# Performance work log

Hardware: AMD Instinct MI355X
Metric: run time of the kernel (lower is better)

The kernel has to match this reference:

```python
import jax, jax.numpy as jnp
import numpy as np

NUM_CLASSES = 21
IOU_THRESH = 0.5
NEG_POS_RATIO = 3
VAR0, VAR1 = 0.1, 0.2


def point_form(priors):
    # (cx,cy,w,h) -> (xmin,ymin,xmax,ymax)
    return jnp.concatenate([priors[:, :2] - priors[:, 2:] / 2,
                            priors[:, :2] + priors[:, 2:] / 2], axis=-1)


def jaccard(box_a, box_b):
    # box_a: [n,4] point form, box_b: [N,4] point form -> [n,N]
    max_xy = jnp.minimum(box_a[:, None, 2:], box_b[None, :, 2:])
    min_xy = jnp.maximum(box_a[:, None, :2], box_b[None, :, :2])
    inter = jnp.prod(jnp.clip(max_xy - min_xy, 0.0, None), axis=-1)
    area_a = jnp.prod(box_a[:, 2:] - box_a[:, :2], axis=-1)[:, None]
    area_b = jnp.prod(box_b[:, 2:] - box_b[:, :2], axis=-1)[None, :]
    return inter / (area_a + area_b - inter)


def encode(matched, priors):
    # matched: [N,4] point form, priors: [N,4] center form
    g_cxcy = ((matched[:, :2] + matched[:, 2:]) / 2 - priors[:, :2]) / (VAR0 * priors[:, 2:])
    g_wh = jnp.log((matched[:, 2:] - matched[:, :2]) / priors[:, 2:]) / VAR1
    return jnp.concatenate([g_cxcy, g_wh], axis=-1)


def match_one(truths, labels, priors):
    # truths: [n_obj,4], labels: [n_obj], priors: [N,4] center form
    ov = jaccard(truths, point_form(priors))          # [n_obj, N]
    best_prior_idx = jnp.argmax(ov, axis=1)           # [n_obj]
    best_truth_overlap = jnp.max(ov, axis=0)          # [N]
    best_truth_idx = jnp.argmax(ov, axis=0)           # [N]
    best_truth_overlap = best_truth_overlap.at[best_prior_idx].set(2.0)
    def body(j, bti):
        return bti.at[best_prior_idx[j]].set(j)
    best_truth_idx = jax.lax.fori_loop(0, truths.shape[0], body, best_truth_idx)
    matched = truths[best_truth_idx]                  # [N,4]
    conf = labels[best_truth_idx].astype(jnp.int32) + 1
    conf = jnp.where(best_truth_overlap < IOU_THRESH, 0, conf)
    return encode(matched, priors), conf


def smooth_l1(x):
    ax = jnp.abs(x)
    return jnp.where(ax < 1.0, 0.5 * x * x, ax - 0.5)


def setup_inputs() -> dict:
    key = jax.random.key(0)
    k1, k2, k3, k4, k5, k6, k7 = jax.random.split(key, 7)
    B, N, n_obj = 128, 8732, 16
    loc_data = jax.random.normal(k1, (B, N, 4), jnp.float32)
    conf_data = jax.random.normal(k2, (B, N, NUM_CLASSES), jnp.float32)
    # valid ground-truth boxes in [0,1], point form, plus class label in [0,20)
    mins = jax.random.uniform(k3, (B, n_obj, 2)) * 0.6
    sizes = jax.random.uniform(k4, (B, n_obj, 2)) * 0.35 + 0.05
    labels = jax.random.randint(k5, (B, n_obj), 0, NUM_CLASSES - 1).astype(jnp.float32)
    targets = jnp.concatenate([mins, mins + sizes, labels[..., None]], axis=-1)
    # priors in center form with positive w,h
    centers = jax.random.uniform(k6, (N, 2))
    wh = jax.random.uniform(k7, (N, 2)) * 0.5 + 0.05
    priors = jnp.concatenate([centers, wh], axis=-1).astype(jnp.float32)
    return {"loc_data": loc_data, "conf_data": conf_data, "targets": targets, "priors": priors}


def _forward(loc_data, conf_data, targets, priors):
    B, N = loc_data.shape[0], loc_data.shape[1]
    truths, labels = targets[:, :, :4], targets[:, :, 4]
    target_loc, target_conf = jax.vmap(match_one, in_axes=(0, 0, None))(truths, labels, priors)
    pos = target_conf > 0                             # [B,N]
    # localization: smooth-L1 summed over positive priors
    loss_l = jnp.sum(smooth_l1(loc_data - target_loc) * pos[..., None].astype(loc_data.dtype))
    # per-prior CE surrogate: logsumexp - logit[target]
    lse = jax.nn.logsumexp(conf_data, axis=-1)        # [B,N]
    gathered = jnp.take_along_axis(conf_data, target_conf[..., None], axis=-1)[..., 0]
    loss_c_all = lse - gathered                       # [B,N]
    # hard negative mining via double argsort ranking (positives excluded)
    lc = jnp.where(pos, 0.0, loss_c_all)
    loss_idx = jnp.argsort(-lc, axis=1)
    idx_rank = jnp.argsort(loss_idx, axis=1)
    num_pos = jnp.sum(pos.astype(jnp.int32), axis=1, keepdims=True)   # [B,1]
    num_neg = jnp.minimum(NEG_POS_RATIO * num_pos, N - 1)
    neg = idx_rank < num_neg
    sel = pos | neg
    loss_c = jnp.sum(jnp.where(sel, loss_c_all, 0.0))
    n_total = jnp.sum(num_pos).astype(loc_data.dtype)
    return loss_l / n_total, loss_c / n_total


def reference(loc_data, conf_data, targets, priors):
    return _forward(loc_data, conf_data, targets, priors)
```

## Files before the change

### kernel.cpp

```cpp
#include <hip/hip_runtime.h>
#include <cstdint>
#include <cstddef>

#define HB1 4096
#define HB2 2048
#define CMAX 21
#define IOU_T 0.5f

__device__ __forceinline__ float sl1(float x) {
    float ax = fabsf(x);
    return ax < 1.0f ? 0.5f * x * x : ax - 0.5f;
}

__global__ __launch_bounds__(256) void kA_best_prior(
    const float* __restrict__ targets, const float* __restrict__ priors,
    float* __restrict__ bpi_val, int* __restrict__ bpi_idx,
    int* __restrict__ num_pos_g, float* __restrict__ accB_g,
    float* __restrict__ acc_g, unsigned* __restrict__ done_g,
    int N, int NOBJ, int SLICES, int CHUNK, int B)
{
    const int s = blockIdx.x, b = blockIdx.y, t = threadIdx.x;
    __shared__ float tb[16 * 4];
    __shared__ float ta[16];
    __shared__ float wv[4 * 16];
    __shared__ int   wi[4 * 16];

    if (s == 0 && b == 0) {
        for (int q = t; q < B; q += 256) num_pos_g[q] = 0;
        for (int q = t; q < 2 * B; q += 256) accB_g[q] = 0.f;
        if (t < 4) acc_g[t] = 0.f;
        if (t == 0) *done_g = 0u;
    }

    if (t < 16) {
        if (t < NOBJ) {
            const float* tr = targets + ((size_t)b * NOBJ + t) * 5;
            float x0 = tr[0], y0 = tr[1], x1 = tr[2], y1 = tr[3];
            tb[t * 4 + 0] = x0; tb[t * 4 + 1] = y0;
            tb[t * 4 + 2] = x1; tb[t * 4 + 3] = y1;
            ta[t] = (x1 - x0) * (y1 - y0);
        } else {
            tb[t * 4 + 0] = 0.f; tb[t * 4 + 1] = 0.f;
            tb[t * 4 + 2] = 0.f; tb[t * 4 + 3] = 0.f;
            ta[t] = 0.f;
        }
    }
    __syncthreads();

    float bv[16]; int bi[16];
#pragma unroll
    for (int j = 0; j < 16; j++) { bv[j] = -1.0f; bi[j] = 0x7fffffff; }

    const int start = s * CHUNK;
    const int end = min(start + CHUNK, N);
    for (int i = start + t; i < end; i += 256) {
        float4 p = ((const float4*)priors)[i];
        float bx0 = p.x - p.z * 0.5f, by0 = p.y - p.w * 0.5f;
        float bx1 = p.x + p.z * 0.5f, by1 = p.y + p.w * 0.5f;
        float ab = (bx1 - bx0) * (by1 - by0);
#pragma unroll
        for (int j = 0; j < 16; j++) {
            float iw = fminf(tb[j * 4 + 2], bx1) - fmaxf(tb[j * 4 + 0], bx0);
            float ih = fminf(tb[j * 4 + 3], by1) - fmaxf(tb[j * 4 + 1], by0);
            iw = fmaxf(iw, 0.f); ih = fmaxf(ih, 0.f);
            float inter = iw * ih;
            float iou = inter / (ta[j] + ab - inter);
            if (iou > bv[j] || (iou == bv[j] && i < bi[j])) { bv[j] = iou; bi[j] = i; }
        }
    }

#pragma unroll
    for (int off = 32; off >= 1; off >>= 1) {
#pragma unroll
        for (int j = 0; j < 16; j++) {
            float v2 = __shfl_down(bv[j], off, 64);
            int   i2 = __shfl_down(bi[j], off, 64);
            if (v2 > bv[j] || (v2 == bv[j] && i2 < bi[j])) { bv[j] = v2; bi[j] = i2; }
        }
    }
    const int wid = t >> 6, lane = t & 63;
    if (lane == 0) {
#pragma unroll
        for (int j = 0; j < 16; j++) { wv[wid * 16 + j] = bv[j]; wi[wid * 16 + j] = bi[j]; }
    }
    __syncthreads();
    if (t < 16) {
        float v = wv[t]; int idx = wi[t];
#pragma unroll
        for (int w = 1; w < 4; w++) {
            float v2 = wv[w * 16 + t]; int i2 = wi[w * 16 + t];
            if (v2 > v || (v2 == v && i2 < idx)) { v = v2; idx = i2; }
        }
        if (t < NOBJ) {
            int o = (b * SLICES + s) * 16 + t;
            bpi_val[o] = v;
            bpi_idx[o] = idx;
        }
    }
}

#define IOU_STEP(j) { \
    float4 tj = tb4[j]; \
    float taj = (tj.z - tj.x) * (tj.w - tj.y); \
    float iw = fminf(tj.z, bx1) - fmaxf(tj.x, bx0); \
    float ih = fminf(tj.w, by1) - fmaxf(tj.y, by0); \
    iw = fmaxf(iw, 0.f); ih = fmaxf(ih, 0.f); \
    float inter = iw * ih; \
    float iou = inter * __builtin_amdgcn_rcpf(taj + ab - inter); \
    if (iou > bto) { bto = iou; bti = (j); } }

__global__ __launch_bounds__(256, 3) void kB_main(
    const float* __restrict__ loc, const float* __restrict__ conf,
    const float* __restrict__ targets, const float* __restrict__ priors,
    const float* __restrict__ bpi_val, const int* __restrict__ bpi_idx,
    float* __restrict__ lc_out, int* __restrict__ num_pos, float* __restrict__ accB,
    int N, int NOBJ, int SLICES, int TPB, int BPB)
{
    const int g = blockIdx.x;
    const int b = g / BPB;
    const int j0 = g % BPB;
    const int t = threadIdx.x;
    const int wid = t >> 6, lane = t & 63;

    __shared__ __align__(16) float buf[256 * CMAX];
    __shared__ __align__(16) float tb[16 * 4];
    __shared__ float tl[16];
    __shared__ __align__(16) int bpi_s[16];
    __shared__ float wred[4 * 3];

    if (t < 16) {
        if (t < NOBJ) {
            const float* tr = targets + ((size_t)b * NOBJ + t) * 5;
            tb[t * 4 + 0] = tr[0]; tb[t * 4 + 1] = tr[1];
            tb[t * 4 + 2] = tr[2]; tb[t * 4 + 3] = tr[3];
            tl[t] = tr[4];
            float bv = -1.f; int bi = 0x7fffffff;
            for (int s2 = 0; s2 < SLICES; s2++) {
                int o = (b * SLICES + s2) * 16 + t;
                float v = bpi_val[o]; int idx = bpi_idx[o];
                if (v > bv || (v == bv && idx < bi)) { bv = v; bi = idx; }
            }
            bpi_s[t] = bi;
        } else {
            tb[t * 4 + 0] = 0.f; tb[t * 4 + 1] = 0.f; tb[t * 4 + 2] = 0.f; tb[t * 4 + 3] = 0.f;
            tl[t] = 0.f; bpi_s[t] = -1;
        }
    }

    const float* confB = conf + (size_t)b * N * CMAX;
    const float* locB  = loc + (size_t)b * N * 4;

    float4 r0, r1, r2, r3, r4, r5, pld, ppr;

    auto stage = [&](int xx) {
        int i0s = xx * 256;
        int rows_s = min(256, N - i0s);
        int nf4s = (rows_s * CMAX) >> 2;
        const float4* s4 = (const float4*)(confB + (size_t)i0s * CMAX);
        if (t + 0    < nf4s) r0 = s4[t + 0];
        if (t + 256  < nf4s) r1 = s4[t + 256];
        if (t + 512  < nf4s) r2 = s4[t + 512];
        if (t + 768  < nf4s) r3 = s4[t + 768];
        if (t + 1024 < nf4s) r4 = s4[t + 1024];
        if (t + 1280 < nf4s) r5 = s4[t + 1280];
        if (t < rows_s) {
            ppr = ((const float4*)priors)[i0s + t];
            pld = ((const float4*)locB)[i0s + t];
        }
    };

    float ll = 0.f, plc = 0.f, np = 0.f;
    int x = j0;
    if (x < TPB) stage(x);

    while (x < TPB) {
        const int i0 = x * 256;
        const int rows = min(256, N - i0);
        const int nf4 = (rows * CMAX) >> 2;

        __syncthreads();

        float4 myp = ppr, myl = pld;
        float4* bp4f = (float4*)buf;
        if (t + 0    < nf4) bp4f[t + 0]    = r0;
        if (t + 256  < nf4) bp4f[t + 256]  = r1;
        if (t + 512  < nf4) bp4f[t + 512]  = r2;
        if (t + 768  < nf4) bp4f[t + 768]  = r3;
        if (t + 1024 < nf4) bp4f[t + 1024] = r4;
        if (t + 1280 < nf4) bp4f[t + 1280] = r5;
        __syncthreads();

        int xn = x + BPB;
        if (xn < TPB) stage(xn);

        if (t < rows) {
            const int i = i0 + t;
            float4 pp = myp;
            float bx0 = pp.x - pp.z * 0.5f, by0 = pp.y - pp.w * 0.5f;
            float bx1 = pp.x + pp.z * 0.5f, by1 = pp.y + pp.w * 0.5f;
            float ab = (bx1 - bx0) * (by1 - by0);
            float bto = -1.f; int bti = 0;
            const float4* tb4 = (const float4*)tb;
            if (NOBJ == 16) {
#pragma unroll
                for (int j = 0; j < 16; j++) IOU_STEP(j);
            } else {
                for (int j = 0; j < NOBJ; j++) IOU_STEP(j);
            }
            const int4* bp4 = (const int4*)bpi_s;
#pragma unroll
            for (int jj = 0; jj < 4; jj++) {
                int4 q = bp4[jj];
                if (q.x == i) { bto = 2.0f; bti = jj * 4 + 0; }
                if (q.y == i) { bto = 2.0f; bti = jj * 4 + 1; }
                if (q.z == i) { bto = 2.0f; bti = jj * 4 + 2; }
                if (q.w == i) { bto = 2.0f; bti = jj * 4 + 3; }
            }
            bool pos = !(bto < IOU_T);
            if (pos) {
                float4 tj = tb4[bti];
                float rz = __builtin_amdgcn_rcpf(pp.z);
                float rw = __builtin_amdgcn_rcpf(pp.w);
                float gcx = ((tj.x + tj.z) * 0.5f - pp.x) * (10.0f * rz);
                float gcy = ((tj.y + tj.w) * 0.5f - pp.y) * (10.0f * rw);
                float gw = __logf((tj.z - tj.x) * rz) * 5.0f;
                float gh = __logf((tj.w - tj.y) * rw) * 5.0f;
                ll += sl1(myl.x - gcx) + sl1(myl.y - gcy) + sl1(myl.z - gw) + sl1(myl.w - gh);
                np += 1.f;
            }
            int cf = pos ? ((int)tl[bti] + 1) : 0;
            const float* cr = buf + t * CMAX;
            float m = cr[0];
#pragma unroll
            for (int c = 1; c < CMAX; c++) m = fmaxf(m, cr[c]);
            float ssum = 0.f;
#pragma unroll
            for (int c = 0; c < CMAX; c++) ssum += __expf(cr[c] - m);
            float lse = m + __logf(ssum);
            float lossc = lse - cr[cf];
            if (pos) plc += lossc;
            float lcv = pos ? 0.f : lossc;
            lcv = fmaxf(lcv, 0.f);
            lc_out[(size_t)b * N + i] = lcv;
        }
        x = xn;
    }

#pragma unroll
    for (int off = 32; off >= 1; off >>= 1) {
        ll  += __shfl_down(ll, off, 64);
        plc += __shfl_down(plc, off, 64);
        np  += __shfl_down(np, off, 64);
    }
    if (lane == 0) { wred[wid * 3 + 0] = ll; wred[wid * 3 + 1] = plc; wred[wid * 3 + 2] = np; }
    __syncthreads();
    if (t == 0) {
        float a0 = 0.f, a1 = 0.f, a2 = 0.f;
#pragma unroll
        for (int w = 0; w < 4; w++) { a0 += wred[w * 3 + 0]; a1 += wred[w * 3 + 1]; a2 += wred[w * 3 + 2]; }
        atomicAdd(&accB[b * 2 + 0], a0);
        atomicAdd(&accB[b * 2 + 1], a1);
        atomicAdd(&num_pos[b], (int)a2);
    }
}

__device__ __forceinline__ void wave_sufscan(int& c, float& s, int lane) {
#pragma unroll
    for (int off = 1; off < 64; off <<= 1) {
        int c2 = __shfl_down(c, off, 64);
        float s2 = __shfl_down(s, off, 64);
        if (lane + off < 64) { c += c2; s += s2; }
    }
}

__global__ __launch_bounds__(1024) void kC_topk(
    const float* __restrict__ lc, const int* __restrict__ num_pos,
    const float* __restrict__ accB,
    float* __restrict__ acc, unsigned* __restrict__ done_ctr,
    float* __restrict__ out, int N, int B)
{
    const int b = blockIdx.x, t = threadIdx.x;
    const int NT = 1024;
    const int wid = t >> 6, lane = t & 63;
    __shared__ __align__(16) int   cnt[HB1];
    __shared__ __align__(16) float sm[HB1];
    __shared__ int   wc[16];
    __shared__ float ws[16];
    __shared__ int s_strad, s_krem;
    __shared__ float s_above;
    __shared__ int s_last;
    __shared__ float wsum[16], wsA[16], wsB[16];

    const int k = min(3 * num_pos[b], N - 1);
    const float* lcb = lc + (size_t)b * N;
    float total = 0.f;

    if (k > 0) {
        ((int4*)cnt)[t] = make_int4(0, 0, 0, 0);
        ((float4*)sm)[t] = make_float4(0.f, 0.f, 0.f, 0.f);
        __syncthreads();
        const int n4 = N >> 2;
        const float4* lcb4 = (const float4*)lcb;
        for (int i = t; i < n4; i += NT) {
            float4 v = lcb4[i];
            { unsigned u = __float_as_uint(v.x) >> 19; atomicAdd(&cnt[u], 1); atomicAdd(&sm[u], v.x); }
            { unsigned u = __float_as_uint(v.y) >> 19; atomicAdd(&cnt[u], 1); atomicAdd(&sm[u], v.y); }
            { unsigned u = __float_as_uint(v.z) >> 19; atomicAdd(&cnt[u], 1); atomicAdd(&sm[u], v.z); }
            { unsigned u = __float_as_uint(v.w) >> 19; atomicAdd(&cnt[u], 1); atomicAdd(&sm[u], v.w); }
        }
        for (int i = (n4 << 2) + t; i < N; i += NT) {
            float v = lcb[i];
            unsigned u = __float_as_uint(v) >> 19;
            atomicAdd(&cnt[u], 1); atomicAdd(&sm[u], v);
        }
        __syncthreads();
        {
            int4  cv = ((const int4*)cnt)[t];
            float4 sv = ((const float4*)sm)[t];
            int   ci = cv.x + cv.y + cv.z + cv.w;
            float si = sv.x + sv.y + sv.z + sv.w;
            wave_sufscan(ci, si, lane);
            if (lane == 0) { wc[wid] = ci; ws[wid] = si; }
            __syncthreads();
            int cab = 0; float sab = 0.f;
            for (int w = wid + 1; w < 16; w++) { cab += wc[w]; sab += ws[w]; }
            int   i0c = ci + cab;          float f0 = si + sab;
            int   i1c = i0c - cv.x;        float f1 = f0 - sv.x;
            int   i2c = i1c - cv.y;        float f2 = f1 - sv.y;
            int   i3c = i2c - cv.z;        float f3 = f2 - sv.z;
            int   i4c = i3c - cv.w;
            if (i1c < k && k <= i0c) { s_strad = 4 * t + 0; s_krem = k - i1c; s_above = f1; }
            if (i2c < k && k <= i1c) { s_strad = 4 * t + 1; s_krem = k - i2c; s_above = f2; }
            if (i3c < k && k <= i2c) { s_strad = 4 * t + 2; s_krem = k - i3c; s_above = f3; }
            if (i4c < k && k <= i3c) { s_strad = 4 * t + 3; s_krem = k - i4c; s_above = f3 - sv.w; }
        }
        __syncthreads();
        const int s1 = s_strad, k2 = s_krem;
        total += s_above;

        __syncthreads();
        ((int2*)cnt)[t] = make_int2(0, 0);
        ((float2*)sm)[t] = make_float2(0.f, 0.f);
        __syncthreads();
        for (int i = t; i < N; i += NT) {
            float v = lcb[i];
            unsigned u = __float_as_uint(v);
            if ((int)(u >> 19) == s1) {
                int q = (int)((u >> 8) & 0x7FF);
                atomicAdd(&cnt[q], 1); atomicAdd(&sm[q], v);
            }
        }
        __syncthreads();
        {
            int2  cv = ((const int2*)cnt)[t];
            float2 sv = ((const float2*)sm)[t];
            int   ci = cv.x + cv.y;
            float si = sv.x + sv.y;
            wave_sufscan(ci, si, lane);
            if (lane == 0) { wc[wid] = ci; ws[wid] = si; }
            __syncthreads();
            int cab = 0; float sab = 0.f;
            for (int w = wid + 1; w < 16; w++) { cab += wc[w]; sab += ws[w]; }
            int   i0c = ci + cab;       float f0 = si + sab;
            int   i1c = i0c - cv.x;     float f1 = f0 - sv.x;
            int   i2c = i1c - cv.y;
            if (i1c < k2 && k2 <= i0c) { s_strad = 2 * t + 0; s_krem = k2 - i1c; s_above = f1; }
            if (i2c < k2 && k2 <= i1c) { s_strad = 2 * t + 1; s_krem = k2 - i2c; s_above = f1 - sv.y; }
        }
        __syncthreads();
        const int s2 = s_strad, krem = s_krem;
        total += s_above;
        float tval = __uint_as_float((((unsigned)s1) << 19) | (((unsigned)s2) << 8));
        total += (float)krem * tval;
    }

    if (t == 0) {
        if (k > 0) atomicAdd(&acc[1], total);
        __threadfence();
        unsigned old = atomicAdd(done_ctr, 1u);
        s_last = (old == (unsigned)gridDim.x - 1u) ? 1 : 0;
    }
    __syncthreads();
    if (s_last) {
        __threadfence();
        float vn = 0.f, va = 0.f, vb = 0.f;
        for (int q = t; q < B; q += NT) {
            vn += (float)num_pos[q];
            va += accB[q * 2 + 0];
            vb += accB[q * 2 + 1];
        }
#pragma unroll
        for (int off = 32; off >= 1; off >>= 1) {
            vn += __shfl_down(vn, off, 64);
            va += __shfl_down(va, off, 64);
            vb += __shfl_down(vb, off, 64);
        }
        if (lane == 0) { wsum[wid] = vn; wsA[wid] = va; wsB[wid] = vb; }
        __syncthreads();
        if (t == 0) {
            float n = 0.f, a = 0.f, bsum = 0.f;
#pragma unroll
            for (int w = 0; w < 16; w++) { n += wsum[w]; a += wsA[w]; bsum += wsB[w]; }
            float l2 = atomicAdd(&acc[1], 0.0f);
            out[0] = a / n;
            out[1] = (bsum + l2) / n;
        }
    }
}

extern "C" void kernel_launch(void* const* d_in, const int* in_sizes, int n_in,
                              void* d_out, int out_size, void* d_ws, size_t ws_size,
                              hipStream_t stream)
{
    const float* loc     = (const float*)d_in[0];
    const float* conf    = (const float*)d_in[1];
    const float* targets = (const float*)d_in[2];
    const float* priors  = (const float*)d_in[3];
    float* out = (float*)d_out;

    const int N = in_sizes[3] / 4;
    const int BN = in_sizes[0] / 4;
    const int B = BN / N;
    const int NOBJ = in_sizes[2] / (B * 5);
    const int SLICES = 8;
    const int CHUNK = (N + SLICES - 1) / SLICES;
    const int TPB = (N + 255) / 256;
    const int BPB = 14;

    char* w = (char*)d_ws;
    float*    lc_ws   = (float*)w;                         size_t off = (size_t)BN * 4;
    float*    bpi_val = (float*)(w + off);                 off += (size_t)B * SLICES * 16 * 4;
    int*      bpi_idx = (int*)(w + off);                   off += (size_t)B * SLICES * 16 * 4;
    int*      num_pos = (int*)(w + off);                   off += (size_t)B * 4;
    float*    accB    = (float*)(w + off);                 off += (size_t)B * 2 * 4;
    float*    acc     = (float*)(w + off);                 off += 16;
    unsigned* done    = (unsigned*)(w + off);              off += 16;

    dim3 gA(SLICES, B);
    kA_best_prior<<<gA, 256, 0, stream>>>(targets, priors, bpi_val, bpi_idx,
                                          num_pos, accB, acc, done, N, NOBJ, SLICES, CHUNK, B);

    kB_main<<<B * BPB, 256, 0, stream>>>(loc, conf, targets, priors, bpi_val, bpi_idx,
                                         lc_ws, num_pos, accB, N, NOBJ, SLICES, TPB, BPB);

    kC_topk<<<B, 1024, 0, stream>>>(lc_ws, num_pos, accB, acc, done, out, N, B);
}
```

Baseline: 228.7 us.

## Fuse top-k selection into main kernel via per-batch last-block completion counter

The separate histogram-based top-k kernel is merged into the main loss kernel. The last of the BPB blocks of each batch row, found through an atomic per-batch counter, runs the two-pass radix selection with 256 threads instead of 1024. This removes one kernel launch and the gap between launches, and lets selection for one row overlap with main work on other rows. The change also lowers BPB from 14 to 8, raises the occupancy hint to 4 blocks per CU, and puts shared memory into a 32KB union. The tail work per row now runs on a single 256-thread block, so that serial stage may get longer.

After: 390.4 us. 70.7% more time.

```diff
diff --git a/kernel.cpp b/kernel.cpp
--- a/kernel.cpp
+++ b/kernel.cpp
@@ -2,8 +2,6 @@
 #include <cstdint>
 #include <cstddef>
 
-#define HB1 4096
-#define HB2 2048
 #define CMAX 21
 #define IOU_T 0.5f
 
@@ -17,6 +15,7 @@
     float* __restrict__ bpi_val, int* __restrict__ bpi_idx,
     int* __restrict__ num_pos_g, float* __restrict__ accB_g,
     float* __restrict__ acc_g, unsigned* __restrict__ done_g,
+    int* __restrict__ bdone_g,
     int N, int NOBJ, int SLICES, int CHUNK, int B)
 {
     const int s = blockIdx.x, b = blockIdx.y, t = threadIdx.x;
@@ -28,6 +27,7 @@
     if (s == 0 && b == 0) {
         for (int q = t; q < B; q += 256) num_pos_g[q] = 0;
         for (int q = t; q < 2 * B; q += 256) accB_g[q] = 0.f;
+        for (int q = t; q < B; q += 256) bdone_g[q] = 0;
         if (t < 4) acc_g[t] = 0.f;
         if (t == 0) *done_g = 0u;
     }
@@ -99,6 +99,15 @@
     }
 }
 
+__device__ __forceinline__ void wave_sufscan(int& c, float& s, int lane) {
+#pragma unroll
+    for (int off = 1; off < 64; off <<= 1) {
+        int c2 = __shfl_down(c, off, 64);
+        float s2 = __shfl_down(s, off, 64);
+        if (lane + off < 64) { c += c2; s += s2; }
+    }
+}
+
 #define IOU_STEP(j) { \
     float4 tj = tb4[j]; \
     float taj = (tj.z - tj.x) * (tj.w - tj.y); \
@@ -109,12 +118,19 @@
     float iou = inter * __builtin_amdgcn_rcpf(taj + ab - inter); \
     if (iou > bto) { bto = iou; bti = (j); } }
 
-__global__ __launch_bounds__(256, 3) void kB_main(
+#define CSTEP(idx, cc, ff, kk) { \
+    int nc = curc - (cc); float nf = curf - (ff); \
+    if (nc < (kk) && (kk) <= curc) { s_strad = (idx); s_krem = (kk) - nc; s_above = nf; } \
+    curc = nc; curf = nf; }
+
+__global__ __launch_bounds__(256, 4) void kBC_main(
     const float* __restrict__ loc, const float* __restrict__ conf,
     const float* __restrict__ targets, const float* __restrict__ priors,
     const float* __restrict__ bpi_val, const int* __restrict__ bpi_idx,
     float* __restrict__ lc_out, int* __restrict__ num_pos, float* __restrict__ accB,
-    int N, int NOBJ, int SLICES, int TPB, int BPB)
+    int* __restrict__ bdone, float* __restrict__ acc, unsigned* __restrict__ done_ctr,
+    float* __restrict__ out,
+    int N, int NOBJ, int SLICES, int TPB, int BPB, int B)
 {
     const int g = blockIdx.x;
     const int b = g / BPB;
@@ -122,11 +138,20 @@
     const int t = threadIdx.x;
     const int wid = t >> 6, lane = t & 63;
 
-    __shared__ __align__(16) float buf[256 * CMAX];
+    __shared__ __align__(16) char smem[32768];
     __shared__ __align__(16) float tb[16 * 4];
     __shared__ float tl[16];
     __shared__ __align__(16) int bpi_s[16];
     __shared__ float wred[4 * 3];
+    __shared__ int s_go;
+    __shared__ int wc[4];
+    __shared__ float ws[4];
+    __shared__ int s_strad, s_krem;
+    __shared__ float s_above;
+    __shared__ int s_last;
+    __shared__ float wsum[4], wsA[4], wsB[4];
+
+    float* buf = (float*)smem;
 
     if (t < 16) {
         if (t < NOBJ) {
@@ -262,87 +287,80 @@
         atomicAdd(&accB[b * 2 + 1], a1);
         atomicAdd(&num_pos[b], (int)a2);
     }
-}
-
-__device__ __forceinline__ void wave_sufscan(int& c, float& s, int lane) {
-#pragma unroll
-    for (int off = 1; off < 64; off <<= 1) {
-        int c2 = __shfl_down(c, off, 64);
-        float s2 = __shfl_down(s, off, 64);
-        if (lane + off < 64) { c += c2; s += s2; }
-    }
-}
-
-__global__ __launch_bounds__(1024) void kC_topk(
-    const float* __restrict__ lc, const int* __restrict__ num_pos,
-    const float* __restrict__ accB,
-    float* __restrict__ acc, unsigned* __restrict__ done_ctr,
-    float* __restrict__ out, int N, int B)
-{
-    const int b = blockIdx.x, t = threadIdx.x;
-    const int NT = 1024;
-    const int wid = t >> 6, lane = t & 63;
-    __shared__ __align__(16) int   cnt[HB1];
-    __shared__ __align__(16) float sm[HB1];
-    __shared__ int   wc[16];
-    __shared__ float ws[16];
-    __shared__ int s_strad, s_krem;
-    __shared__ float s_above;
-    __shared__ int s_last;
-    __shared__ float wsum[16], wsA[16], wsB[16];
-
+
+    __threadfence();
+    if (t == 0) {
+        int old = atomicAdd(&bdone[b], 1);
+        s_go = (old == BPB - 1) ? 1 : 0;
+    }
+    __syncthreads();
+    if (!s_go) return;
+    __threadfence();
+
+    int*   cnt = (int*)smem;
+    float* sm  = (float*)(smem + 16384);
     const int k = min(3 * num_pos[b], N - 1);
-    const float* lcb = lc + (size_t)b * N;
+    const float* lcb = lc_out + (size_t)b * N;
     float total = 0.f;
 
     if (k > 0) {
-        ((int4*)cnt)[t] = make_int4(0, 0, 0, 0);
-        ((float4*)sm)[t] = make_float4(0.f, 0.f, 0.f, 0.f);
+#pragma unroll
+        for (int q = 0; q < 4; q++) {
+            ((int4*)cnt)[t + 256 * q] = make_int4(0, 0, 0, 0);
+            ((float4*)sm)[t + 256 * q] = make_float4(0.f, 0.f, 0.f, 0.f);
+        }
         __syncthreads();
         const int n4 = N >> 2;
         const float4* lcb4 = (const float4*)lcb;
-        for (int i = t; i < n4; i += NT) {
+        for (int i = t; i < n4; i += 256) {
             float4 v = lcb4[i];
             { unsigned u = __float_as_uint(v.x) >> 19; atomicAdd(&cnt[u], 1); atomicAdd(&sm[u], v.x); }
             { unsigned u = __float_as_uint(v.y) >> 19; atomicAdd(&cnt[u], 1); atomicAdd(&sm[u], v.y); }
             { unsigned u = __float_as_uint(v.z) >> 19; atomicAdd(&cnt[u], 1); atomicAdd(&sm[u], v.z); }
             { unsigned u = __float_as_uint(v.w) >> 19; atomicAdd(&cnt[u], 1); atomicAdd(&sm[u], v.w); }
         }
-        for (int i = (n4 << 2) + t; i < N; i += NT) {
+        for (int i = (n4 << 2) + t; i < N; i += 256) {
             float v = lcb[i];
             unsigned u = __float_as_uint(v) >> 19;
             atomicAdd(&cnt[u], 1); atomicAdd(&sm[u], v);
         }
         __syncthreads();
         {
-            int4  cv = ((const int4*)cnt)[t];
-            float4 sv = ((const float4*)sm)[t];
-            int   ci = cv.x + cv.y + cv.z + cv.w;
-            float si = sv.x + sv.y + sv.z + sv.w;
+            int4   cv0 = ((const int4*)cnt)[4 * t + 0], cv1 = ((const int4*)cnt)[4 * t + 1];
+            int4   cv2 = ((const int4*)cnt)[4 * t + 2], cv3 = ((const int4*)cnt)[4 * t + 3];
+            float4 sv0 = ((const float4*)sm)[4 * t + 0], sv1 = ((const float4*)sm)[4 * t + 1];
+            float4 sv2 = ((const float4*)sm)[4 * t + 2], sv3 = ((const float4*)sm)[4 * t + 3];
+            int ci = cv0.x + cv0.y + cv0.z + cv0.w + cv1.x + cv1.y + cv1.z + cv1.w
+                   + cv2.x + cv2.y + cv2.z + cv2.w + cv3.x + cv3.y + cv3.z + cv3.w;
+            float si = sv0.x + sv0.y + sv0.z + sv0.w + sv1.x + sv1.y + sv1.z + sv1.w
+                     + sv2.x + sv2.y + sv2.z + sv2.w + sv3.x + sv3.y + sv3.z + sv3.w;
             wave_sufscan(ci, si, lane);
             if (lane == 0) { wc[wid] = ci; ws[wid] = si; }
             __syncthreads();
             int cab = 0; float sab = 0.f;
-            for (int w = wid + 1; w < 16; w++) { cab += wc[w]; sab += ws[w]; }
-            int   i0c = ci + cab;          float f0 = si + sab;
-            int   i1c = i0c - cv.x;        float f1 = f0 - sv.x;
-            int   i2c = i1c - cv.y;        float f2 = f1 - sv.y;
-            int   i3c = i2c - cv.z;        float f3 = f2 - sv.z;
-            int   i4c = i3c - cv.w;
-            if (i1c < k && k <= i0c) { s_strad = 4 * t + 0; s_krem = k - i1c; s_above = f1; }
-            if (i2c < k && k <= i1c) { s_strad = 4 * t + 1; s_krem = k - i2c; s_above = f2; }
-            if (i3c < k && k <= i2c) { s_strad = 4 * t + 2; s_krem = k - i3c; s_above = f3; }
-            if (i4c < k && k <= i3c) { s_strad = 4 * t + 3; s_krem = k - i4c; s_above = f3 - sv.w; }
+            for (int w = wid + 1; w < 4; w++) { cab += wc[w]; sab += ws[w]; }
+            int curc = ci + cab; float curf = si + sab;
+            const int base = 16 * t;
+            CSTEP(base + 0,  cv0.x, sv0.x, k) CSTEP(base + 1,  cv0.y, sv0.y, k)
+            CSTEP(base + 2,  cv0.z, sv0.z, k) CSTEP(base + 3,  cv0.w, sv0.w, k)
+            CSTEP(base + 4,  cv1.x, sv1.x, k) CSTEP(base + 5,  cv1.y, sv1.y, k)
+            CSTEP(base + 6,  cv1.z, sv1.z, k) CSTEP(base + 7,  cv1.w, sv1.w, k)
+            CSTEP(base + 8,  cv2.x, sv2.x, k) CSTEP(base + 9,  cv2.y, sv2.y, k)
+            CSTEP(base + 10, cv2.z, sv2.z, k) CSTEP(base + 11, cv2.w, sv2.w, k)
+            CSTEP(base + 12, cv3.x, sv3.x, k) CSTEP(base + 13, cv3.y, sv3.y, k)
+            CSTEP(base + 14, cv3.z, sv3.z, k) CSTEP(base + 15, cv3.w, sv3.w, k)
         }
         __syncthreads();
         const int s1 = s_strad, k2 = s_krem;
         total += s_above;
 
         __syncthreads();
-        ((int2*)cnt)[t] = make_int2(0, 0);
-        ((float2*)sm)[t] = make_float2(0.f, 0.f);
-        __syncthreads();
-        for (int i = t; i < N; i += NT) {
+        ((int4*)cnt)[t] = make_int4(0, 0, 0, 0);
+        ((int4*)cnt)[t + 256] = make_int4(0, 0, 0, 0);
+        ((float4*)sm)[t] = make_float4(0.f, 0.f, 0.f, 0.f);
+        ((float4*)sm)[t + 256] = make_float4(0.f, 0.f, 0.f, 0.f);
+        __syncthreads();
+        for (int i = t; i < N; i += 256) {
             float v = lcb[i];
             unsigned u = __float_as_uint(v);
             if ((int)(u >> 19) == s1) {
@@ -352,20 +370,21 @@
         }
         __syncthreads();
         {
-            int2  cv = ((const int2*)cnt)[t];
-            float2 sv = ((const float2*)sm)[t];
-            int   ci = cv.x + cv.y;
-            float si = sv.x + sv.y;
+            int4   cv0 = ((const int4*)cnt)[2 * t + 0], cv1 = ((const int4*)cnt)[2 * t + 1];
+            float4 sv0 = ((const float4*)sm)[2 * t + 0], sv1 = ((const float4*)sm)[2 * t + 1];
+            int ci = cv0.x + cv0.y + cv0.z + cv0.w + cv1.x + cv1.y + cv1.z + cv1.w;
+            float si = sv0.x + sv0.y + sv0.z + sv0.w + sv1.x + sv1.y + sv1.z + sv1.w;
             wave_sufscan(ci, si, lane);
             if (lane == 0) { wc[wid] = ci; ws[wid] = si; }
             __syncthreads();
             int cab = 0; float sab = 0.f;
-            for (int w = wid + 1; w < 16; w++) { cab += wc[w]; sab += ws[w]; }
-            int   i0c = ci + cab;       float f0 = si + sab;
-            int   i1c = i0c - cv.x;     float f1 = f0 - sv.x;
-            int   i2c = i1c - cv.y;
-            if (i1c < k2 && k2 <= i0c) { s_strad = 2 * t + 0; s_krem = k2 - i1c; s_above = f1; }
-            if (i2c < k2 && k2 <= i1c) { s_strad = 2 * t + 1; s_krem = k2 - i2c; s_above = f1 - sv.y; }
+            for (int w = wid + 1; w < 4; w++) { cab += wc[w]; sab += ws[w]; }
+            int curc = ci + cab; float curf = si + sab;
+            const int base = 8 * t;
+            CSTEP(base + 0, cv0.x, sv0.x, k2) CSTEP(base + 1, cv0.y, sv0.y, k2)
+            CSTEP(base + 2, cv0.z, sv0.z, k2) CSTEP(base + 3, cv0.w, sv0.w, k2)
+            CSTEP(base + 4, cv1.x, sv1.x, k2) CSTEP(base + 5, cv1.y, sv1.y, k2)
+            CSTEP(base + 6, cv1.z, sv1.z, k2) CSTEP(base + 7, cv1.w, sv1.w, k2)
         }
         __syncthreads();
         const int s2 = s_strad, krem = s_krem;
@@ -378,13 +397,13 @@
         if (k > 0) atomicAdd(&acc[1], total);
         __threadfence();
         unsigned old = atomicAdd(done_ctr, 1u);
-        s_last = (old == (unsigned)gridDim.x - 1u) ? 1 : 0;
+        s_last = (old == (unsigned)(B - 1)) ? 1 : 0;
     }
     __syncthreads();
     if (s_last) {
         __threadfence();
         float vn = 0.f, va = 0.f, vb = 0.f;
-        for (int q = t; q < B; q += NT) {
+        for (int q = t; q < B; q += 256) {
             vn += (float)num_pos[q];
             va += accB[q * 2 + 0];
             vb += accB[q * 2 + 1];
@@ -400,7 +419,7 @@
         if (t == 0) {
             float n = 0.f, a = 0.f, bsum = 0.f;
 #pragma unroll
-            for (int w = 0; w < 16; w++) { n += wsum[w]; a += wsA[w]; bsum += wsB[w]; }
+            for (int w = 0; w < 4; w++) { n += wsum[w]; a += wsA[w]; bsum += wsB[w]; }
             float l2 = atomicAdd(&acc[1], 0.0f);
             out[0] = a / n;
             out[1] = (bsum + l2) / n;
@@ -425,7 +444,7 @@
     const int SLICES = 8;
     const int CHUNK = (N + SLICES - 1) / SLICES;
     const int TPB = (N + 255) / 256;
-    const int BPB = 14;
+    const int BPB = 8;
 
     char* w = (char*)d_ws;
     float*    lc_ws   = (float*)w;                         size_t off = (size_t)BN * 4;
@@ -433,15 +452,16 @@
     int*      bpi_idx = (int*)(w + off);                   off += (size_t)B * SLICES * 16 * 4;
     int*      num_pos = (int*)(w + off);                   off += (size_t)B * 4;
     float*    accB    = (float*)(w + off);                 off += (size_t)B * 2 * 4;
+    int*      bdone   = (int*)(w + off);                   off += (size_t)B * 4;
     float*    acc     = (float*)(w + off);                 off += 16;
     unsigned* done    = (unsigned*)(w + off);              off += 16;
 
     dim3 gA(SLICES, B);
     kA_best_prior<<<gA, 256, 0, stream>>>(targets, priors, bpi_val, bpi_idx,
-                                          num_pos, accB, acc, done, N, NOBJ, SLICES, CHUNK, B);
-
-    kB_main<<<B * BPB, 256, 0, stream>>>(loc, conf, targets, priors, bpi_val, bpi_idx,
-                                         lc_ws, num_pos, accB, N, NOBJ, SLICES, TPB, BPB);
-
-    kC_topk<<<B, 1024, 0, stream>>>(lc_ws, num_pos, accB, acc, done, out, N, B);
+                                          num_pos, accB, acc, done, bdone,
+                                          N, NOBJ, SLICES, CHUNK, B);
+
+    kBC_main<<<B * BPB, 256, 0, stream>>>(loc, conf, targets, priors, bpi_val, bpi_idx,
+                                          lc_ws, num_pos, accB, bdone, acc, done, out,
+                                          N, NOBJ, SLICES, TPB, BPB, B);
 }
```

## Process two prior rows per thread with 512-row tiles in main kernel

Applied to the files above, without the earlier changes.

The main matching/loss kernel now stages 512 prior rows per tile instead of 256, so each thread handles two rows. The IoU, encode and logsumexp work for both rows is interleaved to raise instruction-level parallelism. Blocks per batch drop from 14 to 6, which halves the number of tile iterations and barriers per row. In exchange the kernel uses more staging registers and twice the shared memory per block, which may cut occupancy. The generic NOBJ fallback loop is dropped, so the IoU loop is hard-coded to 16 objects.

Result: no change. 229.4 us (+0.3%).

```diff
diff --git a/kernel.cpp b/kernel.cpp
--- a/kernel.cpp
+++ b/kernel.cpp
@@ -99,15 +99,15 @@
     }
 }
 
-#define IOU_STEP(j) { \
+#define IOU_STEP2(j, P, BX0, BY0, BX1, BY1, AB, BTO, BTI) { \
     float4 tj = tb4[j]; \
     float taj = (tj.z - tj.x) * (tj.w - tj.y); \
-    float iw = fminf(tj.z, bx1) - fmaxf(tj.x, bx0); \
-    float ih = fminf(tj.w, by1) - fmaxf(tj.y, by0); \
+    float iw = fminf(tj.z, BX1) - fmaxf(tj.x, BX0); \
+    float ih = fminf(tj.w, BY1) - fmaxf(tj.y, BY0); \
     iw = fmaxf(iw, 0.f); ih = fmaxf(ih, 0.f); \
     float inter = iw * ih; \
-    float iou = inter * __builtin_amdgcn_rcpf(taj + ab - inter); \
-    if (iou > bto) { bto = iou; bti = (j); } }
+    float iou = inter * __builtin_amdgcn_rcpf(taj + AB - inter); \
+    if (iou > BTO) { BTO = iou; BTI = (j); } }
 
 __global__ __launch_bounds__(256, 3) void kB_main(
     const float* __restrict__ loc, const float* __restrict__ conf,
@@ -122,7 +122,7 @@
     const int t = threadIdx.x;
     const int wid = t >> 6, lane = t & 63;
 
-    __shared__ __align__(16) float buf[256 * CMAX];
+    __shared__ __align__(16) float buf[512 * CMAX];
     __shared__ __align__(16) float tb[16 * 4];
     __shared__ float tl[16];
     __shared__ __align__(16) int bpi_s[16];
@@ -150,22 +150,32 @@
     const float* confB = conf + (size_t)b * N * CMAX;
     const float* locB  = loc + (size_t)b * N * 4;
 
-    float4 r0, r1, r2, r3, r4, r5, pld, ppr;
+    float4 r0, r1, r2, r3, r4, r5, r6, r7, r8, r9, r10;
+    float4 pr0, pr1, ld0, ld1;
 
     auto stage = [&](int xx) {
-        int i0s = xx * 256;
-        int rows_s = min(256, N - i0s);
+        int i0s = xx * 512;
+        int rows_s = min(512, N - i0s);
         int nf4s = (rows_s * CMAX) >> 2;
         const float4* s4 = (const float4*)(confB + (size_t)i0s * CMAX);
-        if (t + 0    < nf4s) r0 = s4[t + 0];
-        if (t + 256  < nf4s) r1 = s4[t + 256];
-        if (t + 512  < nf4s) r2 = s4[t + 512];
-        if (t + 768  < nf4s) r3 = s4[t + 768];
-        if (t + 1024 < nf4s) r4 = s4[t + 1024];
-        if (t + 1280 < nf4s) r5 = s4[t + 1280];
+        if (t + 0    < nf4s) r0  = s4[t + 0];
+        if (t + 256  < nf4s) r1  = s4[t + 256];
+        if (t + 512  < nf4s) r2  = s4[t + 512];
+        if (t + 768  < nf4s) r3  = s4[t + 768];
+        if (t + 1024 < nf4s) r4  = s4[t + 1024];
+        if (t + 1280 < nf4s) r5  = s4[t + 1280];
+        if (t + 1536 < nf4s) r6  = s4[t + 1536];
+        if (t + 1792 < nf4s) r7  = s4[t + 1792];
+        if (t + 2048 < nf4s) r8  = s4[t + 2048];
+        if (t + 2304 < nf4s) r9  = s4[t + 2304];
+        if (t + 2560 < nf4s) r10 = s4[t + 2560];
         if (t < rows_s) {
-            ppr = ((const float4*)priors)[i0s + t];
-            pld = ((const float4*)locB)[i0s + t];
+            pr0 = ((const float4*)priors)[i0s + t];
+            ld0 = ((const float4*)locB)[i0s + t];
+        }
+        if (256 + t < rows_s) {
+            pr1 = ((const float4*)priors)[i0s + 256 + t];
+            ld1 = ((const float4*)locB)[i0s + 256 + t];
         }
     };
 
@@ -174,13 +184,13 @@
     if (x < TPB) stage(x);
 
     while (x < TPB) {
-        const int i0 = x * 256;
-        const int rows = min(256, N - i0);
+        const int i0 = x * 512;
+        const int rows = min(512, N - i0);
         const int nf4 = (rows * CMAX) >> 2;
 
         __syncthreads();
 
-        float4 myp = ppr, myl = pld;
+        float4 myp0 = pr0, myl0 = ld0, myp1 = pr1, myl1 = ld1;
         float4* bp4f = (float4*)buf;
         if (t + 0    < nf4) bp4f[t + 0]    = r0;
         if (t + 256  < nf4) bp4f[t + 256]  = r1;
@@ -188,60 +198,101 @@
         if (t + 768  < nf4) bp4f[t + 768]  = r3;
         if (t + 1024 < nf4) bp4f[t + 1024] = r4;
         if (t + 1280 < nf4) bp4f[t + 1280] = r5;
+        if (t + 1536 < nf4) bp4f[t + 1536] = r6;
+        if (t + 1792 < nf4) bp4f[t + 1792] = r7;
+        if (t + 2048 < nf4) bp4f[t + 2048] = r8;
+        if (t + 2304 < nf4) bp4f[t + 2304] = r9;
+        if (t + 2560 < nf4) bp4f[t + 2560] = r10;
         __syncthreads();
 
         int xn = x + BPB;
         if (xn < TPB) stage(xn);
 
-        if (t < rows) {
-            const int i = i0 + t;
-            float4 pp = myp;
-            float bx0 = pp.x - pp.z * 0.5f, by0 = pp.y - pp.w * 0.5f;
-            float bx1 = pp.x + pp.z * 0.5f, by1 = pp.y + pp.w * 0.5f;
-            float ab = (bx1 - bx0) * (by1 - by0);
-            float bto = -1.f; int bti = 0;
-            const float4* tb4 = (const float4*)tb;
-            if (NOBJ == 16) {
-#pragma unroll
-                for (int j = 0; j < 16; j++) IOU_STEP(j);
-            } else {
-                for (int j = 0; j < NOBJ; j++) IOU_STEP(j);
+        const bool a0 = (t < rows);
+        const bool a1 = (256 + t < rows);
+        const int i1 = i0 + t, i2 = i0 + 256 + t;
+        const float4* tb4 = (const float4*)tb;
+        const int4* bp4 = (const int4*)bpi_s;
+
+        float bto0 = -1.f, bto1 = -1.f; int bti0 = 0, bti1 = 0;
+        float bx00 = 0, by00 = 0, bx10 = 0, by10 = 0, ab0 = 0;
+        float bx01 = 0, by01 = 0, bx11 = 0, by11 = 0, ab1 = 0;
+        if (a0) {
+            bx00 = myp0.x - myp0.z * 0.5f; by00 = myp0.y - myp0.w * 0.5f;
+            bx10 = myp0.x + myp0.z * 0.5f; by10 = myp0.y + myp0.w * 0.5f;
+            ab0 = (bx10 - bx00) * (by10 - by00);
+        }
+        if (a1) {
+            bx01 = myp1.x - myp1.z * 0.5f; by01 = myp1.y - myp1.w * 0.5f;
+            bx11 = myp1.x + myp1.z * 0.5f; by11 = myp1.y + myp1.w * 0.5f;
+            ab1 = (bx11 - bx01) * (by11 - by01);
+        }
+#pragma unroll
+        for (int j = 0; j < 16; j++) {
+            IOU_STEP2(j, 0, bx00, by00, bx10, by10, ab0, bto0, bti0);
+            IOU_STEP2(j, 1, bx01, by01, bx11, by11, ab1, bto1, bti1);
+        }
+#pragma unroll
+        for (int jj = 0; jj < 4; jj++) {
+            int4 q = bp4[jj];
+            if (q.x == i1) { bto0 = 2.0f; bti0 = jj * 4 + 0; }
+            if (q.y == i1) { bto0 = 2.0f; bti0 = jj * 4 + 1; }
+            if (q.z == i1) { bto0 = 2.0f; bti0 = jj * 4 + 2; }
+            if (q.w == i1) { bto0 = 2.0f; bti0 = jj * 4 + 3; }
+            if (q.x == i2) { bto1 = 2.0f; bti1 = jj * 4 + 0; }
+            if (q.y == i2) { bto1 = 2.0f; bti1 = jj * 4 + 1; }
+            if (q.z == i2) { bto1 = 2.0f; bti1 = jj * 4 + 2; }
+            if (q.w == i2) { bto1 = 2.0f; bti1 = jj * 4 + 3; }
+        }
+        bool pos0 = a0 && !(bto0 < IOU_T);
+        bool pos1 = a1 && !(bto1 < IOU_T);
+        if (pos0) {
+            float4 tj = tb4[bti0];
+            float rz = __builtin_amdgcn_rcpf(myp0.z);
+            float rw = __builtin_amdgcn_rcpf(myp0.w);
+            float gcx = ((tj.x + tj.z) * 0.5f - myp0.x) * (10.0f * rz);
+            float gcy = ((tj.y + tj.w) * 0.5f - myp0.y) * (10.0f * rw);
+            float gw = __logf((tj.z - tj.x) * rz) * 5.0f;
+            float gh = __logf((tj.w - tj.y) * rw) * 5.0f;
+            ll += sl1(myl0.x - gcx) + sl1(myl0.y - gcy) + sl1(myl0.z - gw) + sl1(myl0.w - gh);
+            np += 1.f;
+        }
+        if (pos1) {
+            float4 tj = tb4[bti1];
+            float rz = __builtin_amdgcn_rcpf(myp1.z);
+            float rw = __builtin_amdgcn_rcpf(myp1.w);
+            float gcx = ((tj.x + tj.z) * 0.5f - myp1.x) * (10.0f * rz);
+            float gcy = ((tj.y + tj.w) * 0.5f - myp1.y) * (10.0f * rw);
+            float gw = __logf((tj.z - tj.x) * rz) * 5.0f;
+            float gh = __logf((tj.w - tj.y) * rw) * 5.0f;
+            ll += sl1(myl1.x - gcx) + sl1(myl1.y - gcy) + sl1(myl1.z - gw) + sl1(myl1.w - gh);
+            np += 1.f;
+        }
+        {
+            int cf0 = pos0 ? ((int)tl[bti0] + 1) : 0;
+            int cf1 = pos1 ? ((int)tl[bti1] + 1) : 0;
+            const float* cr0 = buf + t * CMAX;
+            const float* cr1 = buf + (256 + t) * CMAX;
+            float m0 = cr0[0], m1 = cr1[0];
+#pragma unroll
+            for (int c = 1; c < CMAX; c++) { m0 = fmaxf(m0, cr0[c]); m1 = fmaxf(m1, cr1[c]); }
+            float s0 = 0.f, s1 = 0.f;
+#pragma unroll
+            for (int c = 0; c < CMAX; c++) { s0 += __expf(cr0[c] - m0); s1 += __expf(cr1[c] - m1); }
+            float lse0 = m0 + __logf(s0);
+            float lse1 = m1 + __logf(s1);
+            if (a0) {
+                float lossc = lse0 - cr0[cf0];
+                if (pos0) plc += lossc;
+                float lcv = pos0 ? 0.f : lossc;
+                lc_out[(size_t)b * N + i1] = fmaxf(lcv, 0.f);
             }
-            const int4* bp4 = (const int4*)bpi_s;
-#pragma unroll
-            for (int jj = 0; jj < 4; jj++) {
-                int4 q = bp4[jj];
-                if (q.x == i) { bto = 2.0f; bti = jj * 4 + 0; }
-                if (q.y == i) { bto = 2.0f; bti = jj * 4 + 1; }
-                if (q.z == i) { bto = 2.0f; bti = jj * 4 + 2; }
-                if (q.w == i) { bto = 2.0f; bti = jj * 4 + 3; }
+            if (a1) {
+                float lossc = lse1 - cr1[cf1];
+                if (pos1) plc += lossc;
+                float lcv = pos1 ? 0.f : lossc;
+                lc_out[(size_t)b * N + i2] = fmaxf(lcv, 0.f);
             }
-            bool pos = !(bto < IOU_T);
-            if (pos) {
-                float4 tj = tb4[bti];
-                float rz = __builtin_amdgcn_rcpf(pp.z);
-                float rw = __builtin_amdgcn_rcpf(pp.w);
-                float gcx = ((tj.x + tj.z) * 0.5f - pp.x) * (10.0f * rz);
-                float gcy = ((tj.y + tj.w) * 0.5f - pp.y) * (10.0f * rw);
-                float gw = __logf((tj.z - tj.x) * rz) * 5.0f;
-                float gh = __logf((tj.w - tj.y) * rw) * 5.0f;
-                ll += sl1(myl.x - gcx) + sl1(myl.y - gcy) + sl1(myl.z - gw) + sl1(myl.w - gh);
-                np += 1.f;
-            }
-            int cf = pos ? ((int)tl[bti] + 1) : 0;
-            const float* cr = buf + t * CMAX;
-            float m = cr[0];
-#pragma unroll
-            for (int c = 1; c < CMAX; c++) m = fmaxf(m, cr[c]);
-            float ssum = 0.f;
-#pragma unroll
-            for (int c = 0; c < CMAX; c++) ssum += __expf(cr[c] - m);
-            float lse = m + __logf(ssum);
-            float lossc = lse - cr[cf];
-            if (pos) plc += lossc;
-            float lcv = pos ? 0.f : lossc;
-            lcv = fmaxf(lcv, 0.f);
-            lc_out[(size_t)b * N + i] = lcv;
         }
         x = xn;
     }
@@ -255,12 +306,12 @@
     if (lane == 0) { wred[wid * 3 + 0] = ll; wred[wid * 3 + 1] = plc; wred[wid * 3 + 2] = np; }
     __syncthreads();
     if (t == 0) {
-        float a0 = 0.f, a1 = 0.f, a2 = 0.f;
-#pragma unroll
-        for (int w = 0; w < 4; w++) { a0 += wred[w * 3 + 0]; a1 += wred[w * 3 + 1]; a2 += wred[w * 3 + 2]; }
-        atomicAdd(&accB[b * 2 + 0], a0);
-        atomicAdd(&accB[b * 2 + 1], a1);
-        atomicAdd(&num_pos[b], (int)a2);
+        float a0r = 0.f, a1r = 0.f, a2r = 0.f;
+#pragma unroll
+        for (int w = 0; w < 4; w++) { a0r += wred[w * 3 + 0]; a1r += wred[w * 3 + 1]; a2r += wred[w * 3 + 2]; }
+        atomicAdd(&accB[b * 2 + 0], a0r);
+        atomicAdd(&accB[b * 2 + 1], a1r);
+        atomicAdd(&num_pos[b], (int)a2r);
     }
 }
 
@@ -424,8 +475,8 @@
     const int NOBJ = in_sizes[2] / (B * 5);
     const int SLICES = 8;
     const int CHUNK = (N + SLICES - 1) / SLICES;
-    const int TPB = (N + 255) / 256;
-    const int BPB = 14;
+    const int TPB = (N + 511) / 512;
+    const int BPB = 6;
 
     char* w = (char*)d_ws;
     float*    lc_ws   = (float*)w;                         size_t off = (size_t)BN * 4;
```
